# Kernel optimization log

Measured on AMD Instinct MI355X. Metric: run time of the kernel, lower is better.

## Reference

```python
import jax, jax.numpy as jnp
import numpy as np

N_NODES = 20000
N_EDGES = 320000
IN_FEATS = 256
H_FEATS = 256


def setup_inputs() -> dict:
    key = jax.random.key(0)
    ks = jax.random.split(key, 8)
    s = 1.0 / np.sqrt(IN_FEATS)
    return {
        "features": jax.random.normal(ks[0], (N_NODES, IN_FEATS), jnp.float32),
        "src": jax.random.randint(ks[1], (N_EDGES,), 0, N_NODES, jnp.int32),
        "dst": jax.random.randint(ks[2], (N_EDGES,), 0, N_NODES, jnp.int32),
        "W_self1": jax.random.normal(ks[3], (IN_FEATS, H_FEATS), jnp.float32) * s,
        "W_neigh1": jax.random.normal(ks[4], (IN_FEATS, H_FEATS), jnp.float32) * s,
        "b1": jnp.zeros((H_FEATS,), jnp.float32),
        "W_self2": jax.random.normal(ks[5], (H_FEATS, H_FEATS), jnp.float32) * s,
        "W_neigh2": jax.random.normal(ks[6], (H_FEATS, H_FEATS), jnp.float32) * s,
        "b2": jnp.zeros((H_FEATS,), jnp.float32),
    }


def _sage_conv(h, src, dst, W_self, W_neigh, b, n_nodes):
    # mean aggregation of src features onto dst nodes (DGL SAGEConv 'mean')
    msg_sum = jax.ops.segment_sum(h[src], dst, num_segments=n_nodes)  # [N, d]
    deg = jax.ops.segment_sum(jnp.ones_like(dst, dtype=h.dtype), dst,
                              num_segments=n_nodes)  # [N]
    h_neigh = msg_sum / jnp.maximum(deg, 1.0)[:, None]  # isolated nodes -> 0
    return h @ W_self + h_neigh @ W_neigh + b


def reference(features, src, dst, W_self1, W_neigh1, b1, W_self2, W_neigh2, b2):
    n = features.shape[0]
    h = _sage_conv(features, src, dst, W_self1, W_neigh1, b1, n)
    h = jax.nn.relu(h)
    h = _sage_conv(h, src, dst, W_self2, W_neigh2, b2, n)
    # DotPredictor: per-edge dot product of src/dst embeddings
    score = jnp.sum(h[src] * h[dst], axis=1)  # [E]
    return score
```

## Files before the change

kernel.cpp:

```cpp
#include <hip/hip_runtime.h>
#include <hip/hip_bf16.h>
#include <stdint.h>

typedef __bf16 bf16_t;
typedef __bf16 bf16x8 __attribute__((ext_vector_type(8)));
typedef __bf16 bf16x4 __attribute__((ext_vector_type(4)));
typedef float f32x4 __attribute__((ext_vector_type(4)));

#define NFEAT 256
#define KDIM  512
#define BM 64
#define BN 128
#define BK 64

__device__ __forceinline__ void gload_lds16(const void* g, void* l) {
  __builtin_amdgcn_global_load_lds(
      (const __attribute__((address_space(1))) unsigned int*)g,
      (__attribute__((address_space(3))) unsigned int*)l, 16, 0, 0);
}

__device__ int g_flag[256];
__device__ int g_depart;


__global__ void k_count_deg(const int* __restrict__ dst, int* __restrict__ deg, int nE) {
  int i = blockIdx.x * blockDim.x + threadIdx.x;
  if (i < nE) atomicAdd(&deg[dst[i]], 1);
}

__global__ __launch_bounds__(256) void k_scan_fused(const int* __restrict__ deg,
                                                    int* __restrict__ offsets,
                                                    int* __restrict__ cursor,
                                                    float* __restrict__ inv_deg,
                                                    int n, int nb) {
  __shared__ int s[256];
  __shared__ int p[256];
  const int b = blockIdx.x;
  const int tid = threadIdx.x;
  int i = b * 256 + tid;
  int d = (i < n) ? deg[i] : 0;
  s[tid] = d;
  __syncthreads();
  for (int off = 1; off < 256; off <<= 1) {
    int v = (tid >= off) ? s[tid - off] : 0;
    __syncthreads();
    s[tid] += v;
    __syncthreads();
  }
  if (tid == 255) atomicExch(&g_flag[b], s[255] + 1);
  int pv = 0;
  if (tid < b) {
    int v;
    do { v = atomicAdd(&g_flag[tid], 0); } while (v == 0);
    pv = v - 1;
  }
  p[tid] = pv;
  __syncthreads();
  for (int off = 128; off; off >>= 1) {
    if (tid < off) p[tid] += p[tid + off];
    __syncthreads();
  }
  int block_excl = p[0];
  if (i < n) {
    int excl = block_excl + s[tid] - d;
    offsets[i] = excl;
    cursor[i]  = excl;
    inv_deg[i] = 1.0f / (float)(d > 1 ? d : 1);
  }
  __syncthreads();
  if (tid == 0) {
    int old = atomicAdd(&g_depart, 1);
    if (old == nb - 1) {
      for (int j = 0; j < nb; ++j) atomicExch(&g_flag[j], 0);
      atomicExch(&g_depart, 0);
    }
  }
}

__global__ void k_scatter(const int* __restrict__ src, const int* __restrict__ dst,
                          int* __restrict__ cursor, int* __restrict__ csr_src,
                          int2* __restrict__ epack, int nE) {
  int i = blockIdx.x * blockDim.x + threadIdx.x;
  if (i < nE) {
    int d = dst[i];
    int s = src[i];
    int pos = atomicAdd(&cursor[d], 1);
    csr_src[pos] = s;
    epack[pos] = make_int2((d << 16) | s, i);
  }
}

__global__ void k_prep(const float* __restrict__ F,
                       const float* __restrict__ Ws1, const float* __restrict__ Wn1,
                       const float* __restrict__ Ws2, const float* __restrict__ Wn2,
                       bf16_t* __restrict__ WT1, bf16_t* __restrict__ WT2,
                       bf16_t* __restrict__ X,
                       int* __restrict__ deg, int nNodes, int mpad) {
  int t = blockIdx.x * blockDim.x + threadIdx.x;
  if (t < mpad) deg[t] = 0;
  if (t < 2 * NFEAT * KDIM) {
    int layer = t >> 17;
    int r = t & (NFEAT * KDIM - 1);
    int n = r >> 9;
    int k = r & 511;
    const float* Ws = layer ? Ws2 : Ws1;
    const float* Wn = layer ? Wn2 : Wn1;
    float v = (k < NFEAT) ? Ws[k * NFEAT + n] : Wn[(k - NFEAT) * NFEAT + n];
    (layer ? WT2 : WT1)[r] = (bf16_t)v;
  }
  int n = t >> 6;
  int c = (t & 63) * 4;
  if (n < mpad) {
    float4 v = make_float4(0.f, 0.f, 0.f, 0.f);
    if (n < nNodes) v = *(const float4*)&F[(size_t)n * NFEAT + c];
    bf16x4 o;
    o[0] = (bf16_t)v.x; o[1] = (bf16_t)v.y; o[2] = (bf16_t)v.z; o[3] = (bf16_t)v.w;
    *(bf16x4*)&X[(size_t)n * KDIM + c] = o;
  }
}

__global__ __launch_bounds__(256) void k_agg(const bf16_t* __restrict__ Hin,
                                             bf16_t* __restrict__ Hout,
                                             const int* __restrict__ csr_src,
                                             const int* __restrict__ offsets,
                                             const int* __restrict__ deg,
                                             const float* __restrict__ inv_deg,
                                             int instride, int outstride) {
  const int n   = blockIdx.x * 8 + (threadIdx.x >> 5);
  const int l32 = threadIdx.x & 31;
  const int beg = offsets[n];
  const int cnt = deg[n];
  const size_t colo = (size_t)l32 * 8;

  float acc[8] = {0.f, 0.f, 0.f, 0.f, 0.f, 0.f, 0.f, 0.f};

  int s[4];
  #pragma unroll
  for (int q = 0; q < 4; ++q) s[q] = (q < cnt) ? csr_src[beg + q] : -1;

  for (int i = 0; i < cnt; i += 4) {
    bf16x8 v[4];
    bool h[4];
    #pragma unroll
    for (int q = 0; q < 4; ++q) {
      h[q] = (s[q] >= 0);
      if (h[q]) v[q] = *(const bf16x8*)&Hin[(size_t)s[q] * instride + colo];
    }
    #pragma unroll
    for (int q = 0; q < 4; ++q) {
      int j = i + 4 + q;
      s[q] = (j < cnt) ? csr_src[beg + j] : -1;
    }
    #pragma unroll
    for (int q = 0; q < 4; ++q) {
      if (h[q]) {
        #pragma unroll
        for (int e = 0; e < 8; ++e) acc[e] += (float)v[q][e];
      }
    }
  }

  float w = inv_deg[n];
  bf16x8 o;
  #pragma unroll
  for (int e = 0; e < 8; ++e) o[e] = (bf16_t)(acc[e] * w);
  *(bf16x8*)&Hout[(size_t)n * outstride + NFEAT + colo] = o;
}

__global__ __launch_bounds__(256, 3) void k_gemm(const bf16_t* __restrict__ A,
                                                 const bf16_t* __restrict__ BT,
                                                 const float* __restrict__ bias,
                                                 bf16_t* __restrict__ Cout,
                                                 int ostride, int relu) {
  __shared__ __align__(16) bf16_t As[2][BM * BK];
  __shared__ __align__(16) bf16_t Bs[2][BN * BK];
  const int tid  = threadIdx.x;
  const int lane = tid & 63;
  const int wave = tid >> 6;
  const int wr = wave >> 1, wc = wave & 1;
  const int m0 = blockIdx.x * BM;
  const int n0 = blockIdx.y * BN;
  const int l15 = lane & 15;
  const int lk8 = (lane >> 4) * 8;

  f32x4 acc[2][4] = {};

  auto stage = [&](int buf, int kt) {
    const int k0 = kt * BK;
    #pragma unroll
    for (int i = 0; i < 2; ++i) {
      int idx = i * 256 + tid;
      int row = idx >> 3;
      int c8  = (idx & 7) * 8;
      gload_lds16(A + (size_t)(m0 + row) * KDIM + k0 + c8,
                  (char*)&As[buf][0] + (i * 256 + wave * 64) * 16);
    }
    #pragma unroll
    for (int i = 0; i < 4; ++i) {
      int idx = i * 256 + tid;
      int row = idx >> 3;
      int c8  = (idx & 7) * 8;
      gload_lds16(BT + (size_t)(n0 + row) * KDIM + k0 + c8,
                  (char*)&Bs[buf][0] + (i * 256 + wave * 64) * 16);
    }
  };

  auto compute = [&](int buf) {
    #pragma unroll
    for (int kk = 0; kk < 2; ++kk) {
      bf16x8 af[2], bfr[4];
      #pragma unroll
      for (int m = 0; m < 2; ++m) {
        int row = wr * 32 + m * 16 + l15;
        af[m] = *(const bf16x8*)&As[buf][row * BK + kk * 32 + lk8];
      }
      #pragma unroll
      for (int n = 0; n < 4; ++n) {
        int col = wc * 64 + n * 16 + l15;
        bfr[n] = *(const bf16x8*)&Bs[buf][col * BK + kk * 32 + lk8];
      }
      #pragma unroll
      for (int m = 0; m < 2; ++m)
        #pragma unroll
        for (int n = 0; n < 4; ++n)
          acc[m][n] = __builtin_amdgcn_mfma_f32_16x16x32_bf16(af[m], bfr[n], acc[m][n], 0, 0, 0);
    }
  };

  stage(0, 0);
  __syncthreads();
  const int nt = KDIM / BK;
  int cur = 0;
  for (int t = 0; t < nt; ++t) {
    if (t + 1 < nt) stage(cur ^ 1, t + 1);
    compute(cur);
    __syncthreads();
    cur ^= 1;
  }

  #pragma unroll
  for (int n = 0; n < 4; ++n) {
    int col = n0 + wc * 64 + n * 16 + l15;
    float bv = bias[col];
    #pragma unroll
    for (int m = 0; m < 2; ++m) {
      int rbase = m0 + wr * 32 + m * 16 + (lane >> 4) * 4;
      #pragma unroll
      for (int j = 0; j < 4; ++j) {
        float v = acc[m][n][j] + bv;
        if (relu) v = fmaxf(v, 0.f);
        Cout[(size_t)(rbase + j) * ostride + col] = (bf16_t)v;
      }
    }
  }
}

__global__ __launch_bounds__(256) void k_edge_dot(const bf16_t* __restrict__ H,
                                                  const int2* __restrict__ epack,
                                                  float* __restrict__ out, int nE) {
  const int wid  = (blockIdx.x * blockDim.x + threadIdx.x) >> 6;
  const int lane = threadIdx.x & 63;
  const int l15  = lane & 15;
  const int hi   = lane >> 4;
  const int e0   = wid * 16;
  if (e0 >= nE) return;
  int pos = e0 + l15;
  if (pos >= nE) pos = nE - 1;

  const int2 e = epack[pos];
  const int s = e.x & 0xFFFF;
  const int d = ((unsigned)e.x) >> 16;
  const bf16_t* ps = H + (size_t)s * NFEAT + hi * 8;
  const bf16_t* pd = H + (size_t)d * NFEAT + hi * 8;

  f32x4 acc = {0.f, 0.f, 0.f, 0.f};
  #pragma unroll
  for (int ks = 0; ks < 8; ++ks) {
    bf16x8 a = *(const bf16x8*)(ps + ks * 32);
    bf16x8 b = *(const bf16x8*)(pd + ks * 32);
    acc = __builtin_amdgcn_mfma_f32_16x16x32_bf16(a, b, acc, 0, 0, 0);
  }

  if ((l15 >> 2) == hi && (e0 + l15) < nE) {
    int j = l15 & 3;
    float v = acc[0];
    v = (j == 1) ? acc[1] : v;
    v = (j == 2) ? acc[2] : v;
    v = (j == 3) ? acc[3] : v;
    out[e.y] = v;
  }
}


extern "C" void kernel_launch(void* const* d_in, const int* in_sizes, int n_in,
                              void* d_out, int out_size, void* d_ws, size_t ws_size,
                              hipStream_t stream) {
  const float* features = (const float*)d_in[0];
  const int*   src      = (const int*)d_in[1];
  const int*   dst      = (const int*)d_in[2];
  const float* Wself1   = (const float*)d_in[3];
  const float* Wneigh1  = (const float*)d_in[4];
  const float* b1       = (const float*)d_in[5];
  const float* Wself2   = (const float*)d_in[6];
  const float* Wneigh2  = (const float*)d_in[7];
  const float* b2       = (const float*)d_in[8];
  float* score = (float*)d_out;

  const int nNodes = in_sizes[0] / NFEAT;
  const int nE     = in_sizes[1];
  const int mpad   = ((nNodes + 127) / 128) * 128;

  char* ws = (char*)d_ws;
  size_t off = 0;
  auto alloc = [&](size_t bytes) { char* p = ws + off; off += (bytes + 255) & ~(size_t)255; return p; };
  bf16_t* Xcat1   = (bf16_t*)alloc((size_t)mpad * KDIM * 2);
  bf16_t* Xcat2   = (bf16_t*)alloc((size_t)mpad * KDIM * 2);
  bf16_t* H2      = (bf16_t*)alloc((size_t)mpad * NFEAT * 2);
  bf16_t* WT1     = (bf16_t*)alloc((size_t)NFEAT * KDIM * 2);
  bf16_t* WT2     = (bf16_t*)alloc((size_t)NFEAT * KDIM * 2);
  int*    deg     = (int*)alloc((size_t)mpad * 4);
  int*    offsets = (int*)alloc((size_t)mpad * 4);
  int*    cursor  = (int*)alloc((size_t)mpad * 4);
  float*  inv_deg = (float*)alloc((size_t)mpad * 4);
  int*    csr_src = (int*)alloc((size_t)nE * 4);
  int2*   epack   = (int2*)alloc((size_t)nE * 8);

  const int eb = (nE + 255) / 256;
  const int nb = (mpad + 255) / 256;

  k_prep<<<(mpad * 64 + 255) / 256, 256, 0, stream>>>(features, Wself1, Wneigh1,
                                                      Wself2, Wneigh2, WT1, WT2,
                                                      Xcat1, deg, nNodes, mpad);

  k_count_deg<<<eb, 256, 0, stream>>>(dst, deg, nE);
  k_scan_fused<<<nb, 256, 0, stream>>>(deg, offsets, cursor, inv_deg, mpad, nb);
  k_scatter<<<eb, 256, 0, stream>>>(src, dst, cursor, csr_src, epack, nE);

  k_agg<<<mpad / 8, 256, 0, stream>>>(Xcat1, Xcat1, csr_src, offsets, deg, inv_deg, KDIM, KDIM);
  dim3 ggrid(mpad / BM, NFEAT / BN);
  k_gemm<<<ggrid, 256, 0, stream>>>(Xcat1, WT1, b1, Xcat2, KDIM, 1);

  k_agg<<<mpad / 8, 256, 0, stream>>>(Xcat2, Xcat2, csr_src, offsets, deg, inv_deg, KDIM, KDIM);
  k_gemm<<<ggrid, 256, 0, stream>>>(Xcat2, WT2, b2, H2, NFEAT, 0);

  const int nWaves = (nE + 15) / 16;
  k_edge_dot<<<(nWaves + 3) / 4, 256, 0, stream>>>(H2, epack, score, nE);
}
```

Baseline: 155.8 us.

## Fuse degree count, scan and CSR scatter into one grid-barrier kernel

Merges the three graph-preprocessing kernels (degree counting, prefix scan, edge scatter) into a single persistent kernel of about 79 blocks that uses software grid barriers in global atomics. The aim is to cut two kernel launches and the gaps between them. In exchange, the edge loops now run on far fewer threads in grid-stride fashion, and the spin barriers rely on every block being co-resident on the GPU.

```diff
diff --git a/kernel.cpp b/kernel.cpp
--- a/kernel.cpp
+++ b/kernel.cpp
@@ -19,26 +19,35 @@
       (__attribute__((address_space(3))) unsigned int*)l, 16, 0, 0);
 }
 
-__device__ int g_flag[256];
-__device__ int g_depart;
-
-
-__global__ void k_count_deg(const int* __restrict__ dst, int* __restrict__ deg, int nE) {
-  int i = blockIdx.x * blockDim.x + threadIdx.x;
-  if (i < nE) atomicAdd(&deg[dst[i]], 1);
-}
-
-__global__ __launch_bounds__(256) void k_scan_fused(const int* __restrict__ deg,
-                                                    int* __restrict__ offsets,
-                                                    int* __restrict__ cursor,
-                                                    float* __restrict__ inv_deg,
-                                                    int n, int nb) {
-  __shared__ int s[256];
-  __shared__ int p[256];
-  const int b = blockIdx.x;
+__device__ int g_b1, g_b2, g_b3, g_done;
+__device__ int g_part[128];
+
+__device__ __forceinline__ void grid_bar(int* ctr, int nb) {
+  __syncthreads();
+  if (threadIdx.x == 0) {
+    __threadfence();
+    atomicAdd(ctr, 1);
+    while (atomicAdd(ctr, 0) < nb) { }
+  }
+  __syncthreads();
+}
+
+__global__ __launch_bounds__(256) void k_graph(
+    const int* __restrict__ src, const int* __restrict__ dst,
+    int* __restrict__ deg, int* __restrict__ offsets, int* __restrict__ cursor,
+    float* __restrict__ inv_deg, int* __restrict__ csr_src, int2* __restrict__ epack,
+    int nE, int n, int nb) {
+  const int b   = blockIdx.x;
   const int tid = threadIdx.x;
-  int i = b * 256 + tid;
-  int d = (i < n) ? deg[i] : 0;
+  const int gt  = b * 256 + tid;
+  const int G   = nb * 256;
+
+  for (int e = gt; e < nE; e += G) atomicAdd(&deg[dst[e]], 1);
+  grid_bar(&g_b1, nb);
+
+  __shared__ int s[256], p[256];
+  const int i = b * 256 + tid;
+  const int d = (i < n) ? atomicAdd(&deg[i], 0) : 0;
   s[tid] = d;
   __syncthreads();
   for (int off = 1; off < 256; off <<= 1) {
@@ -47,46 +56,43 @@
     s[tid] += v;
     __syncthreads();
   }
-  if (tid == 255) atomicExch(&g_flag[b], s[255] + 1);
+  if (tid == 255) atomicExch(&g_part[b], s[255]);
+  grid_bar(&g_b2, nb);
+
   int pv = 0;
-  if (tid < b) {
-    int v;
-    do { v = atomicAdd(&g_flag[tid], 0); } while (v == 0);
-    pv = v - 1;
-  }
+  if (tid < b) pv = atomicAdd(&g_part[tid], 0);
   p[tid] = pv;
   __syncthreads();
   for (int off = 128; off; off >>= 1) {
     if (tid < off) p[tid] += p[tid + off];
     __syncthreads();
   }
-  int block_excl = p[0];
+  const int block_excl = p[0];
   if (i < n) {
     int excl = block_excl + s[tid] - d;
     offsets[i] = excl;
-    cursor[i]  = excl;
+    atomicExch(&cursor[i], excl);
     inv_deg[i] = 1.0f / (float)(d > 1 ? d : 1);
   }
+  grid_bar(&g_b3, nb);
+
+  for (int e = gt; e < nE; e += G) {
+    int dd = dst[e];
+    int ss = src[e];
+    int pos = atomicAdd(&cursor[dd], 1);
+    csr_src[pos] = ss;
+    epack[pos] = make_int2((dd << 16) | ss, e);
+  }
+
   __syncthreads();
   if (tid == 0) {
-    int old = atomicAdd(&g_depart, 1);
+    int old = atomicAdd(&g_done, 1);
     if (old == nb - 1) {
-      for (int j = 0; j < nb; ++j) atomicExch(&g_flag[j], 0);
-      atomicExch(&g_depart, 0);
-    }
-  }
-}
-
-__global__ void k_scatter(const int* __restrict__ src, const int* __restrict__ dst,
-                          int* __restrict__ cursor, int* __restrict__ csr_src,
-                          int2* __restrict__ epack, int nE) {
-  int i = blockIdx.x * blockDim.x + threadIdx.x;
-  if (i < nE) {
-    int d = dst[i];
-    int s = src[i];
-    int pos = atomicAdd(&cursor[d], 1);
-    csr_src[pos] = s;
-    epack[pos] = make_int2((d << 16) | s, i);
+      atomicExch(&g_b1, 0);
+      atomicExch(&g_b2, 0);
+      atomicExch(&g_b3, 0);
+      atomicExch(&g_done, 0);
+    }
   }
 }
 
@@ -325,16 +331,14 @@
   int*    csr_src = (int*)alloc((size_t)nE * 4);
   int2*   epack   = (int2*)alloc((size_t)nE * 8);
 
-  const int eb = (nE + 255) / 256;
   const int nb = (mpad + 255) / 256;
 
   k_prep<<<(mpad * 64 + 255) / 256, 256, 0, stream>>>(features, Wself1, Wneigh1,
                                                       Wself2, Wneigh2, WT1, WT2,
                                                       Xcat1, deg, nNodes, mpad);
 
-  k_count_deg<<<eb, 256, 0, stream>>>(dst, deg, nE);
-  k_scan_fused<<<nb, 256, 0, stream>>>(deg, offsets, cursor, inv_deg, mpad, nb);
-  k_scatter<<<eb, 256, 0, stream>>>(src, dst, cursor, csr_src, epack, nE);
+  k_graph<<<nb, 256, 0, stream>>>(src, dst, deg, offsets, cursor, inv_deg,
+                                  csr_src, epack, nE, mpad, nb);
 
   k_agg<<<mpad / 8, 256, 0, stream>>>(Xcat1, Xcat1, csr_src, offsets, deg, inv_deg, KDIM, KDIM);
   dim3 ggrid(mpad / BM, NFEAT / BN);
```

After: 165.8 us. +6.5%, slower.
